# Performance work log

Hardware: AMD Instinct MI355X
Metric: run time of the kernel (lower is better)

Reference implementation:

```python
import jax, jax.numpy as jnp
import numpy as np

D = 69      # input_size = 54 dofs + 15 actions
E = 132     # time2vec embedding
R = 1024    # rnn_size
B = 2048    # batch
S = 50      # source_seq_len
T = 25      # target_seq_len


def setup_inputs() -> dict:
    key = jax.random.key(0)
    ks = jax.random.split(key, 18)
    w = lambda k, shape: jax.random.normal(k, shape, jnp.float32) * 0.05
    return dict(
        encoder_inputs=jax.random.normal(ks[0], (B, S - 1, D), jnp.float32),
        decoder_inputs=jax.random.normal(ks[1], (B, T, D), jnp.float32),
        noise=jax.random.normal(ks[2], (B, R), jnp.float32),
        Wih_enc=w(ks[3], (4 * R, D + E)), Whh_enc=w(ks[4], (4 * R, R)),
        bih_enc=w(ks[5], (4 * R,)), bhh_enc=w(ks[6], (4 * R,)),
        Wih_dec=w(ks[7], (4 * R, D)), Whh_dec=w(ks[8], (4 * R, R)),
        bih_dec=w(ks[9], (4 * R,)), bhh_dec=w(ks[10], (4 * R,)),
        fc1_w=w(ks[11], (D, R)), fc1_b=w(ks[12], (D,)),
        mu_w=w(ks[13], (1, R)), mu_b=w(ks[14], (1,)),
        sigma_w=w(ks[15], (1, R)), sigma_b=jnp.ones((1,), jnp.float32),  # bias 1 keeps sigma away from 0
        t2v_w=w(ks[16], (E, D)), t2v_b=w(ks[17], (E,)),
    )


def _lstm_step(x, h, c, Wih, Whh, bih, bhh):
    # PyTorch LSTMCell gate order: i, f, g, o
    gates = x @ Wih.T + bih + h @ Whh.T + bhh
    i, f, g, o = jnp.split(gates, 4, axis=-1)
    c = jax.nn.sigmoid(f) * c + jax.nn.sigmoid(i) * jnp.tanh(g)
    h = jax.nn.sigmoid(o) * jnp.tanh(c)
    return h, c


def _forward(encoder_inputs, decoder_inputs, noise,
             Wih_enc, Whh_enc, bih_enc, bhh_enc,
             Wih_dec, Whh_dec, bih_dec, bhh_dec,
             fc1_w, fc1_b, mu_w, mu_b, sigma_w, sigma_b, t2v_w, t2v_b):
    batch = encoder_inputs.shape[0]
    # time2vec embedding + concat: [B, S-1, D+E]
    emb = jnp.sin(encoder_inputs @ t2v_w.T + t2v_b)
    enc_seq = jnp.swapaxes(jnp.concatenate([encoder_inputs, emb], axis=2), 0, 1)
    h0 = jnp.zeros((batch, R), encoder_inputs.dtype)
    c0 = jnp.zeros((batch, R), encoder_inputs.dtype)

    def enc_step(carry, x):
        h, c = carry
        h, c = _lstm_step(x, h, c, Wih_enc, Whh_enc, bih_enc, bhh_enc)
        return (h, c), None  # dropout is identity in eval mode

    (h, c), _ = jax.lax.scan(enc_step, (h0, c0), enc_seq)

    mu = h @ mu_w.T + mu_b          # [B, 1]
    sigma = c @ sigma_w.T + sigma_b  # [B, 1]
    h = (h - mu) / sigma
    c = (c - mu) / sigma
    # eval-mode stochastic perturbation (same noise added to both, as in torch)
    h = h + 10.0 * noise
    c = c + 10.0 * noise

    dec_seq = jnp.swapaxes(decoder_inputs, 0, 1)  # [T, B, D]

    def dec_step(carry, x):
        h, c = carry
        h, c = _lstm_step(x, h, c, Wih_dec, Whh_dec, bih_dec, bhh_dec)
        out = x + h @ fc1_w.T + fc1_b  # residual projection
        return (h, c), out

    _, outs = jax.lax.scan(dec_step, (h, c), dec_seq)  # [T, B, D]
    return jnp.swapaxes(outs, 0, 1)  # [B, T, D]


def reference(encoder_inputs, decoder_inputs, noise,
              Wih_enc, Whh_enc, bih_enc, bhh_enc,
              Wih_dec, Whh_dec, bih_dec, bhh_dec,
              fc1_w, fc1_b, mu_w, mu_b, sigma_w, sigma_b, t2v_w, t2v_b):
    return _forward(encoder_inputs, decoder_inputs, noise,
                    Wih_enc, Whh_enc, bih_enc, bhh_enc,
                    Wih_dec, Whh_dec, bih_dec, bhh_dec,
                    fc1_w, fc1_b, mu_w, mu_b, sigma_w, sigma_b, t2v_w, t2v_b)
```

## Files before the change

### kernel.cpp

```cpp
#include <hip/hip_runtime.h>
#include <hip/hip_bf16.h>
#include <math.h>

#define DI 69
#define EE 132
#define RR 1024
#define BB 2048
#define TT 25
#define SE 49

typedef _Float16 f16;
typedef _Float16 v8h __attribute__((ext_vector_type(8)));
typedef float f32x4 __attribute__((ext_vector_type(4)));

__device__ __forceinline__ float sigm(float x) { return 1.0f / (1.0f + __expf(-x)); }
__device__ __forceinline__ float tanhf_fast(float x) {
  float e = __expf(2.0f * x);
  return 1.0f - 2.0f / (e + 1.0f);
}

typedef const __attribute__((address_space(1))) char* gas1p;
typedef __attribute__((address_space(3))) char* las3p;
__device__ __forceinline__ void gld16(const void* g, void* l) {
  __builtin_amdgcn_global_load_lds((gas1p)g, (las3p)l, 16, 0, 0);
}



__global__ void prep_misc_kernel(float* __restrict__ c, f16* __restrict__ h0,
                                 const float* __restrict__ bih_e, const float* __restrict__ bhh_e,
                                 const float* __restrict__ bih_d, const float* __restrict__ bhh_d,
                                 float* __restrict__ bias_e, float* __restrict__ bias_d,
                                 const float* __restrict__ fc1_w, f16* __restrict__ fc1h)
{
  int i = blockIdx.x * 256 + threadIdx.x;
  if (i < BB * RR) { c[i] = 0.0f; h0[i] = (f16)0.0f; }
  if (i < 4096) { bias_e[i] = bih_e[i] + bhh_e[i]; bias_d[i] = bih_d[i] + bhh_d[i]; }
  if (i < 128 * RR) {
    int dr = i >> 10, k = i & 1023;
    int kd = k ^ ((dr & 7) << 3);
    fc1h[(dr << 10) | kd] = (f16)((dr < DI) ? fc1_w[dr * RR + k] : 0.0f);
  }
}

__global__ void prep_wq_kernel(const float* __restrict__ Whh, const float* __restrict__ Wih,
                               f16* __restrict__ Wq, int KT, int DIN)
{
  int j = blockIdx.x;
  int xo = (j & 7) << 3;
  for (int k = threadIdx.x; k < KT; k += blockDim.x) {
    float v;
    if (k < RR) v = Whh[(size_t)j * RR + k];
    else { int kk = k - RR; v = (kk < DIN) ? Wih[(size_t)j * DIN + kk] : 0.0f; }
    Wq[(size_t)j * KT + (k ^ xo)] = (f16)v;
  }
}

__global__ __launch_bounds__(256)
void feat_enc_kernel(const float* __restrict__ enc_in,
                     const float* __restrict__ t2v_w, const float* __restrict__ t2v_b,
                     f16* __restrict__ feat)
{
  __shared__ float wl[132 * 100];
  __shared__ float xl[32 * 92];
  __shared__ float bl[132];
  const int tid = threadIdx.x;
  const int t = blockIdx.x >> 6;
  const int b0 = (blockIdx.x & 63) * 32;

  for (int i = tid; i < 132 * 18; i += 256) {
    int e = i / 18, s = i - e * 18, k = s * 4;
    const float* src = t2v_w + e * DI + k;
    float4 v;
    v.x = src[0];
    v.y = (k + 1 < DI) ? src[1] : 0.f;
    v.z = (k + 2 < DI) ? src[2] : 0.f;
    v.w = (k + 3 < DI) ? src[3] : 0.f;
    *(float4*)(wl + e * 100 + k) = v;
  }
  for (int i = tid; i < 32 * 18; i += 256) {
    int r = i / 18, s = i - r * 18, k = s * 4;
    const float* src = enc_in + ((size_t)(b0 + r) * SE + t) * DI + k;
    float4 v;
    v.x = src[0];
    v.y = (k + 1 < DI) ? src[1] : 0.f;
    v.z = (k + 2 < DI) ? src[2] : 0.f;
    v.w = (k + 3 < DI) ? src[3] : 0.f;
    *(float4*)(xl + r * 92 + k) = v;
  }
  if (tid < 132) bl[tid] = t2v_b[tid];
  __syncthreads();

  const int gr = tid >> 5, ge = tid & 31;
  float acc[4][4] = {};
  const float* xr = xl + (gr * 4) * 92;
  for (int k4 = 0; k4 < 18; ++k4) {
    float4 xv[4], wv[4];
    #pragma unroll
    for (int i = 0; i < 4; ++i) xv[i] = *(const float4*)(xr + i * 92 + k4 * 4);
    #pragma unroll
    for (int j = 0; j < 4; ++j) wv[j] = *(const float4*)(wl + (ge + 32 * j) * 100 + k4 * 4);
    #pragma unroll
    for (int i = 0; i < 4; ++i)
      #pragma unroll
      for (int j = 0; j < 4; ++j)
        acc[i][j] += xv[i].x * wv[j].x + xv[i].y * wv[j].y + xv[i].z * wv[j].z + xv[i].w * wv[j].w;
  }
  #pragma unroll
  for (int i = 0; i < 4; ++i) {
    int b = b0 + gr * 4 + i;
    size_t base = ((size_t)t * BB + b) * 256;
    int xo = (b & 7) << 3;
    #pragma unroll
    for (int j = 0; j < 4; ++j) {
      int e = ge + 32 * j;
      feat[base + ((69 + e) ^ xo)] = (f16)__sinf(acc[i][j] + bl[e]);
    }
  }
  if (tid < 32) {
    int b = b0 + tid;
    float a2[4] = {0.f, 0.f, 0.f, 0.f};
    for (int k4 = 0; k4 < 18; ++k4) {
      float4 xv = *(const float4*)(xl + tid * 92 + k4 * 4);
      #pragma unroll
      for (int j = 0; j < 4; ++j) {
        float4 wv = *(const float4*)(wl + (128 + j) * 100 + k4 * 4);
        a2[j] += xv.x * wv.x + xv.y * wv.y + xv.z * wv.z + xv.w * wv.w;
      }
    }
    size_t base = ((size_t)t * BB + b) * 256;
    int xo = (b & 7) << 3;
    #pragma unroll
    for (int j = 0; j < 4; ++j)
      feat[base + ((197 + j) ^ xo)] = (f16)__sinf(a2[j] + bl[128 + j]);
  }
  for (int i = tid; i < 32 * 256; i += 256) {
    int r = i >> 8, k = i & 255;
    if (k >= 69 && k < 201) continue;
    float v = (k < DI) ? xl[r * 92 + k] : 0.f;
    int b = b0 + r;
    feat[((size_t)t * BB + b) * 256 + (k ^ ((b & 7) << 3))] = (f16)v;
  }
}

__global__ void feat_dec_kernel(const float* __restrict__ dec_in, f16* __restrict__ feat)
{
  int idx = blockIdx.x * 256 + threadIdx.x;
  if (idx >= TT * BB * 128) return;
  int k = idx & 127;
  int r = idx >> 7;
  int t = r >> 11, b = r & (BB - 1);
  float v = (k < DI) ? dec_in[(size_t)b * TT * DI + t * DI + k] : 0.0f;
  feat[((size_t)r << 7) | (k ^ ((b & 7) << 3))] = (f16)v;
}

template<int FT, int FPAD, bool WF32>
__global__ __launch_bounds__(256, 2)
void lstm_step_kernel(const f16* __restrict__ hin, const f16* __restrict__ feat,
                      const f16* __restrict__ Wq, const float* __restrict__ bias,
                      float* __restrict__ c, f16* __restrict__ hout,
                      float* __restrict__ hf32)
{
  constexpr int KT = (16 + FT) * 64;
  __shared__ __align__(16) f16 lA[128 * 64];
  __shared__ __align__(16) f16 lB[128 * 64];
  const int tid = threadIdx.x;
  const int m0 = blockIdx.y * 128;
  const int u0 = blockIdx.x * 32;
  const int lane = tid & 63, w = tid >> 6;
  const int wm = w >> 1, wn = w & 1;
  const int lrow = lane & 15;
  const int r8 = lane >> 3, s8 = lane & 7;

  const f16* pA[4]; const f16* pB[4];
  f16* dA[4]; f16* dB[4];
  #pragma unroll
  for (int i = 0; i < 4; ++i) {
    int rA = w * 32 + 8 * i;
    dA[i] = lA + rA * 64;
    dB[i] = lB + rA * 64;
    pA[i] = hin + (size_t)(m0 + rA + r8) * RR + s8 * 8;
    pB[i] = Wq + (size_t)(w * 1024 + u0 + 8 * i + r8) * KT + s8 * 8;
  }

  f32x4 acc[4][4];
  #pragma unroll
  for (int a = 0; a < 4; ++a)
    #pragma unroll
    for (int g = 0; g < 4; ++g) acc[a][g] = (f32x4){0.f, 0.f, 0.f, 0.f};

  const int sw0 = (((lane >> 4)) ^ s8) * 8;
  const int sw1 = (((lane >> 4) | 4) ^ s8) * 8;
  const f16* a0 = lA + (wm * 64 + lrow) * 64 + sw0;
  const f16* a1 = lA + (wm * 64 + lrow) * 64 + sw1;
  const f16* b0 = lB + (wn * 16 + lrow) * 64 + sw0;
  const f16* b1 = lB + (wn * 16 + lrow) * 64 + sw1;

  for (int kt = 0; kt < 16 + FT; ++kt) {
    if (kt == 16) {
      #pragma unroll
      for (int i = 0; i < 4; ++i)
        pA[i] = feat + (size_t)(m0 + w * 32 + 8 * i + r8) * FPAD + s8 * 8;
    }
    #pragma unroll
    for (int i = 0; i < 4; ++i) { gld16(pA[i], dA[i]); pA[i] += 64; }
    #pragma unroll
    for (int i = 0; i < 4; ++i) { gld16(pB[i], dB[i]); pB[i] += 64; }
    __syncthreads();

    v8h av0[4], av1[4], bv0[4], bv1[4];
    #pragma unroll
    for (int mf = 0; mf < 4; ++mf) {
      av0[mf] = *(const v8h*)(a0 + mf * 1024);
      av1[mf] = *(const v8h*)(a1 + mf * 1024);
    }
    #pragma unroll
    for (int g = 0; g < 4; ++g) {
      bv0[g] = *(const v8h*)(b0 + g * 2048);
      bv1[g] = *(const v8h*)(b1 + g * 2048);
    }
    #pragma unroll
    for (int mf = 0; mf < 4; ++mf)
      #pragma unroll
      for (int g = 0; g < 4; ++g) {
        acc[mf][g] = __builtin_amdgcn_mfma_f32_16x16x32_f16(av0[mf], bv0[g], acc[mf][g], 0, 0, 0);
        acc[mf][g] = __builtin_amdgcn_mfma_f32_16x16x32_f16(av1[mf], bv1[g], acc[mf][g], 0, 0, 0);
      }
    __syncthreads();
  }

  const int u = u0 + wn * 16 + lrow;
  const float bi = bias[u], bf = bias[1024 + u], bg = bias[2048 + u], bo = bias[3072 + u];
  #pragma unroll
  for (int mf = 0; mf < 4; ++mf) {
    int rbase = m0 + wm * 64 + mf * 16 + (lane >> 4) * 4;
    #pragma unroll
    for (int q = 0; q < 4; ++q) {
      int r = rbase + q;
      size_t idxc = (size_t)r * RR + u;
      float iv = acc[mf][0][q] + bi;
      float fv = acc[mf][1][q] + bf;
      float gv = acc[mf][2][q] + bg;
      float ov = acc[mf][3][q] + bo;
      float cn = sigm(fv) * c[idxc] + sigm(iv) * tanhf_fast(gv);
      float hn = sigm(ov) * tanhf_fast(cn);
      c[idxc] = cn;
      hout[(size_t)r * RR + (u ^ ((r & 7) << 3))] = (f16)hn;
      if (WF32) hf32[idxc] = hn;
    }
  }
}

__global__ void musigma_kernel(const float* __restrict__ hf, float* __restrict__ c,
                               const float* __restrict__ noise,
                               const float* __restrict__ mu_w, const float* __restrict__ mu_b,
                               const float* __restrict__ sig_w, const float* __restrict__ sig_b,
                               f16* __restrict__ hout)
{
  int b = blockIdx.x, tid = threadIdx.x;
  __shared__ float red[8];
  __shared__ float musig[2];
  float sh = 0.f, sc = 0.f;
  for (int k = tid; k < RR; k += 256) {
    size_t idx = (size_t)b * RR + k;
    sh += hf[idx] * mu_w[k];
    sc += c[idx] * sig_w[k];
  }
  for (int off = 32; off > 0; off >>= 1) { sh += __shfl_down(sh, off); sc += __shfl_down(sc, off); }
  int wid = tid >> 6;
  if ((tid & 63) == 0) { red[wid] = sh; red[4 + wid] = sc; }
  __syncthreads();
  if (tid == 0) {
    musig[0] = red[0] + red[1] + red[2] + red[3] + mu_b[0];
    musig[1] = red[4] + red[5] + red[6] + red[7] + sig_b[0];
  }
  __syncthreads();
  float mu = musig[0], sg = musig[1];
  int xo = (b & 7) << 3;
  for (int k = tid; k < RR; k += 256) {
    size_t idx = (size_t)b * RR + k;
    float n10 = 10.0f * noise[idx];
    float hh = (hf[idx] - mu) / sg + n10;
    float cc = (c[idx] - mu) / sg + n10;
    hout[(size_t)b * RR + (k ^ xo)] = (f16)hh;
    c[idx] = cc;
  }
}

__global__ __launch_bounds__(256, 2)
void final_fc_kernel(const f16* __restrict__ Hd, const f16* __restrict__ fw,
                     const float* __restrict__ fb, const float* __restrict__ dec_in,
                     float* __restrict__ out)
{
  __shared__ __align__(16) f16 lA[128 * 64];
  __shared__ __align__(16) f16 lB[128 * 64];
  const int tid = threadIdx.x;
  const int m0 = blockIdx.x * 128;
  const int lane = tid & 63, w = tid >> 6;
  const int lrow = lane & 15;
  const int r8 = lane >> 3, s8 = lane & 7;

  const f16* pA[4]; const f16* pB[4];
  f16* dA[4]; f16* dB[4];
  #pragma unroll
  for (int i = 0; i < 4; ++i) {
    int rA = w * 32 + 8 * i;
    dA[i] = lA + rA * 64;
    dB[i] = lB + rA * 64;
    pA[i] = Hd + (size_t)(m0 + rA + r8) * RR + s8 * 8;
    pB[i] = fw + (size_t)(rA + r8) * RR + s8 * 8;
  }

  f32x4 acc[2][5];
  #pragma unroll
  for (int a = 0; a < 2; ++a)
    #pragma unroll
    for (int n = 0; n < 5; ++n) acc[a][n] = (f32x4){0.f, 0.f, 0.f, 0.f};

  const int sw0 = (((lane >> 4)) ^ s8) * 8;
  const int sw1 = (((lane >> 4) | 4) ^ s8) * 8;
  const f16* a0 = lA + (w * 32 + lrow) * 64 + sw0;
  const f16* a1 = lA + (w * 32 + lrow) * 64 + sw1;
  const f16* b0 = lB + lrow * 64 + sw0;
  const f16* b1 = lB + lrow * 64 + sw1;

  for (int kt = 0; kt < 16; ++kt) {
    #pragma unroll
    for (int i = 0; i < 4; ++i) { gld16(pA[i], dA[i]); pA[i] += 64; }
    #pragma unroll
    for (int i = 0; i < 4; ++i) { gld16(pB[i], dB[i]); pB[i] += 64; }
    __syncthreads();
    v8h av0[2], av1[2], bv0[5], bv1[5];
    #pragma unroll
    for (int mf = 0; mf < 2; ++mf) {
      av0[mf] = *(const v8h*)(a0 + mf * 1024);
      av1[mf] = *(const v8h*)(a1 + mf * 1024);
    }
    #pragma unroll
    for (int nf = 0; nf < 5; ++nf) {
      bv0[nf] = *(const v8h*)(b0 + nf * 1024);
      bv1[nf] = *(const v8h*)(b1 + nf * 1024);
    }
    #pragma unroll
    for (int mf = 0; mf < 2; ++mf)
      #pragma unroll
      for (int nf = 0; nf < 5; ++nf) {
        acc[mf][nf] = __builtin_amdgcn_mfma_f32_16x16x32_f16(av0[mf], bv0[nf], acc[mf][nf], 0, 0, 0);
        acc[mf][nf] = __builtin_amdgcn_mfma_f32_16x16x32_f16(av1[mf], bv1[nf], acc[mf][nf], 0, 0, 0);
      }
    __syncthreads();
  }
  #pragma unroll
  for (int mf = 0; mf < 2; ++mf) {
    int rbase = m0 + w * 32 + mf * 16 + (lane >> 4) * 4;
    #pragma unroll
    for (int nf = 0; nf < 5; ++nf) {
      int col = nf * 16 + lrow;
      if (col < DI) {
        #pragma unroll
        for (int q = 0; q < 4; ++q) {
          int m = rbase + q;
          int t = m >> 11, b = m & (BB - 1);
          size_t oi = (size_t)b * TT * DI + t * DI + col;
          out[oi] = acc[mf][nf][q] + fb[col] + dec_in[oi];
        }
      }
    }
  }
}

extern "C" void kernel_launch(void* const* d_in, const int* in_sizes, int n_in,
                              void* d_out, int out_size, void* d_ws, size_t ws_size,
                              hipStream_t stream)
{
  const float* enc_in = (const float*)d_in[0];
  const float* dec_in = (const float*)d_in[1];
  const float* noise  = (const float*)d_in[2];
  const float* Wih_e  = (const float*)d_in[3];
  const float* Whh_e  = (const float*)d_in[4];
  const float* bih_e  = (const float*)d_in[5];
  const float* bhh_e  = (const float*)d_in[6];
  const float* Wih_d  = (const float*)d_in[7];
  const float* Whh_d  = (const float*)d_in[8];
  const float* bih_d  = (const float*)d_in[9];
  const float* bhh_d  = (const float*)d_in[10];
  const float* fc1_w  = (const float*)d_in[11];
  const float* fc1_b  = (const float*)d_in[12];
  const float* mu_w   = (const float*)d_in[13];
  const float* mu_b   = (const float*)d_in[14];
  const float* sig_w  = (const float*)d_in[15];
  const float* sig_b  = (const float*)d_in[16];
  const float* t2v_w  = (const float*)d_in[17];
  const float* t2v_b  = (const float*)d_in[18];
  float* outp = (float*)d_out;

  char* ws = (char*)d_ws;
  size_t off = 0;
  auto alloc = [&](size_t bytes) -> char* {
    char* p = ws + off; off += (bytes + 255) & ~(size_t)255; return p;
  };
  f16*   wq_e   = (f16*)alloc((size_t)4096 * 1280 * 2);
  f16*   wq_d   = (f16*)alloc((size_t)4096 * 1152 * 2);
  f16*   fc1h   = (f16*)alloc((size_t)128 * RR * 2);
  float* bias_e = (float*)alloc(4096 * 4);
  float* bias_d = (float*)alloc(4096 * 4);
  f16*   feat_e = (f16*)alloc((size_t)SE * BB * 256 * 2);
  f16*   feat_d = (f16*)alloc((size_t)TT * BB * 128 * 2);
  f16*   h_ping = (f16*)alloc((size_t)BB * RR * 2);
  f16*   h_pong = (f16*)alloc((size_t)BB * RR * 2);
  float* cbuf   = (float*)alloc((size_t)BB * RR * 4);
  float* hf32   = (float*)alloc((size_t)BB * RR * 4);
  f16*   Hd     = (f16*)alloc((size_t)TT * BB * RR * 2);
  if (off > ws_size) return;

  prep_misc_kernel<<<(BB * RR + 255) / 256, 256, 0, stream>>>(
      cbuf, h_ping, bih_e, bhh_e, bih_d, bhh_d, bias_e, bias_d, fc1_w, fc1h);
  prep_wq_kernel<<<4096, 256, 0, stream>>>(Whh_e, Wih_e, wq_e, 1280, DI + EE);
  prep_wq_kernel<<<4096, 256, 0, stream>>>(Whh_d, Wih_d, wq_d, 1152, DI);
  feat_enc_kernel<<<SE * (BB / 32), 256, 0, stream>>>(enc_in, t2v_w, t2v_b, feat_e);
  feat_dec_kernel<<<(TT * BB * 128 + 255) / 256, 256, 0, stream>>>(dec_in, feat_d);

  dim3 sgrid(32, 16, 1);

  f16* hcur = h_ping; f16* hnxt = h_pong;
  for (int t = 0; t < SE; ++t) {
    const f16* ft = feat_e + (size_t)t * BB * 256;
    if (t == SE - 1)
      lstm_step_kernel<4, 256, true><<<sgrid, 256, 0, stream>>>(
          hcur, ft, wq_e, bias_e, cbuf, hnxt, hf32);
    else
      lstm_step_kernel<4, 256, false><<<sgrid, 256, 0, stream>>>(
          hcur, ft, wq_e, bias_e, cbuf, hnxt, nullptr);
    f16* tmp = hcur; hcur = hnxt; hnxt = tmp;
  }

  musigma_kernel<<<BB, 256, 0, stream>>>(hf32, cbuf, noise, mu_w, mu_b, sig_w, sig_b, h_ping);

  const f16* din = h_ping;
  for (int t = 0; t < TT; ++t) {
    f16* hout = Hd + (size_t)t * BB * RR;
    lstm_step_kernel<2, 128, false><<<sgrid, 256, 0, stream>>>(
        din, feat_d + (size_t)t * BB * 128, wq_d, bias_d, cbuf, hout, nullptr);
    din = hout;
  }

  final_fc_kernel<<<(TT * BB) / 128, 256, 0, stream>>>(Hd, fc1h, fc1_b, dec_in, outp);
}
```

Baseline: 2.407 ms.

## Double-buffer LDS tiles in LSTM/fc1 GEMMs and move time2vec onto MFMA

```diff
diff --git a/kernel.cpp b/kernel.cpp
--- a/kernel.cpp
+++ b/kernel.cpp
@@ -31,7 +31,8 @@
                                  const float* __restrict__ bih_e, const float* __restrict__ bhh_e,
                                  const float* __restrict__ bih_d, const float* __restrict__ bhh_d,
                                  float* __restrict__ bias_e, float* __restrict__ bias_d,
-                                 const float* __restrict__ fc1_w, f16* __restrict__ fc1h)
+                                 const float* __restrict__ fc1_w, f16* __restrict__ fc1h,
+                                 const float* __restrict__ t2v_w, f16* __restrict__ wt2)
 {
   int i = blockIdx.x * 256 + threadIdx.x;
   if (i < BB * RR) { c[i] = 0.0f; h0[i] = (f16)0.0f; }
@@ -41,6 +42,11 @@
     int kd = k ^ ((dr & 7) << 3);
     fc1h[(dr << 10) | kd] = (f16)((dr < DI) ? fc1_w[dr * RR + k] : 0.0f);
   }
+  if (i < 160 * 128) {
+    int r = i >> 7, k = i & 127;
+    float v = (r < EE && k < DI) ? t2v_w[r * DI + k] : 0.0f;
+    wt2[(r << 7) | (k ^ ((r & 7) << 3))] = (f16)v;
+  }
 }
 
 __global__ void prep_wq_kernel(const float* __restrict__ Whh, const float* __restrict__ Wih,
@@ -56,90 +62,91 @@
   }
 }
 
+__global__ void xf16_kernel(const float* __restrict__ enc_in,
+                            f16* __restrict__ Xf, f16* __restrict__ feat)
+{
+  int idx = blockIdx.x * 256 + threadIdx.x;
+  if (idx >= SE * BB * 256) return;
+  int j = idx & 255, row = idx >> 8;
+  int t = row >> 11, b = row & (BB - 1);
+  int xo = (b & 7) << 3;
+  int k = j ^ xo;
+  if (k < 128) {
+    float v = (k < DI) ? enc_in[(size_t)b * SE * DI + t * DI + k] : 0.0f;
+    Xf[(size_t)row * 128 + j] = (f16)v;
+    if (k < DI) feat[(size_t)row * 256 + j] = (f16)v;
+  } else if (k >= 201) {
+    feat[(size_t)row * 256 + j] = (f16)0.0f;
+  }
+}
+
 __global__ __launch_bounds__(256)
-void feat_enc_kernel(const float* __restrict__ enc_in,
-                     const float* __restrict__ t2v_w, const float* __restrict__ t2v_b,
-                     f16* __restrict__ feat)
-{
-  __shared__ float wl[132 * 100];
-  __shared__ float xl[32 * 92];
-  __shared__ float bl[132];
+void t2v_kernel(const f16* __restrict__ Xf, const f16* __restrict__ wt2,
+                const float* __restrict__ t2v_b, f16* __restrict__ feat)
+{
+  __shared__ __align__(16) f16 lA[128 * 64];
+  __shared__ __align__(16) f16 lB[160 * 64];
+  __shared__ float bl[EE];
   const int tid = threadIdx.x;
-  const int t = blockIdx.x >> 6;
-  const int b0 = (blockIdx.x & 63) * 32;
-
-  for (int i = tid; i < 132 * 18; i += 256) {
-    int e = i / 18, s = i - e * 18, k = s * 4;
-    const float* src = t2v_w + e * DI + k;
-    float4 v;
-    v.x = src[0];
-    v.y = (k + 1 < DI) ? src[1] : 0.f;
-    v.z = (k + 2 < DI) ? src[2] : 0.f;
-    v.w = (k + 3 < DI) ? src[3] : 0.f;
-    *(float4*)(wl + e * 100 + k) = v;
-  }
-  for (int i = tid; i < 32 * 18; i += 256) {
-    int r = i / 18, s = i - r * 18, k = s * 4;
-    const float* src = enc_in + ((size_t)(b0 + r) * SE + t) * DI + k;
-    float4 v;
-    v.x = src[0];
-    v.y = (k + 1 < DI) ? src[1] : 0.f;
-    v.z = (k + 2 < DI) ? src[2] : 0.f;
-    v.w = (k + 3 < DI) ? src[3] : 0.f;
-    *(float4*)(xl + r * 92 + k) = v;
-  }
-  if (tid < 132) bl[tid] = t2v_b[tid];
-  __syncthreads();
-
-  const int gr = tid >> 5, ge = tid & 31;
-  float acc[4][4] = {};
-  const float* xr = xl + (gr * 4) * 92;
-  for (int k4 = 0; k4 < 18; ++k4) {
-    float4 xv[4], wv[4];
-    #pragma unroll
-    for (int i = 0; i < 4; ++i) xv[i] = *(const float4*)(xr + i * 92 + k4 * 4);
-    #pragma unroll
-    for (int j = 0; j < 4; ++j) wv[j] = *(const float4*)(wl + (ge + 32 * j) * 100 + k4 * 4);
+  const int m0 = blockIdx.x * 128;
+  const int lane = tid & 63, w = tid >> 6;
+  const int lrow = lane & 15;
+  const int r8 = lane >> 3, s8 = lane & 7;
+  if (tid < EE) bl[tid] = t2v_b[tid];
+
+  f32x4 acc[2][10];
+  #pragma unroll
+  for (int a = 0; a < 2; ++a)
+    #pragma unroll
+    for (int n = 0; n < 10; ++n) acc[a][n] = (f32x4){0.f, 0.f, 0.f, 0.f};
+
+  const int sw0 = (((lane >> 4)) ^ s8) * 8;
+  const int sw1 = (((lane >> 4) | 4) ^ s8) * 8;
+
+  for (int kt = 0; kt < 2; ++kt) {
+    __syncthreads();
     #pragma unroll
     for (int i = 0; i < 4; ++i)
-      #pragma unroll
-      for (int j = 0; j < 4; ++j)
-        acc[i][j] += xv[i].x * wv[j].x + xv[i].y * wv[j].y + xv[i].z * wv[j].z + xv[i].w * wv[j].w;
-  }
-  #pragma unroll
-  for (int i = 0; i < 4; ++i) {
-    int b = b0 + gr * 4 + i;
-    size_t base = ((size_t)t * BB + b) * 256;
-    int xo = (b & 7) << 3;
-    #pragma unroll
-    for (int j = 0; j < 4; ++j) {
-      int e = ge + 32 * j;
-      feat[base + ((69 + e) ^ xo)] = (f16)__sinf(acc[i][j] + bl[e]);
-    }
-  }
-  if (tid < 32) {
-    int b = b0 + tid;
-    float a2[4] = {0.f, 0.f, 0.f, 0.f};
-    for (int k4 = 0; k4 < 18; ++k4) {
-      float4 xv = *(const float4*)(xl + tid * 92 + k4 * 4);
-      #pragma unroll
-      for (int j = 0; j < 4; ++j) {
-        float4 wv = *(const float4*)(wl + (128 + j) * 100 + k4 * 4);
-        a2[j] += xv.x * wv.x + xv.y * wv.y + xv.z * wv.z + xv.w * wv.w;
-      }
-    }
-    size_t base = ((size_t)t * BB + b) * 256;
-    int xo = (b & 7) << 3;
-    #pragma unroll
-    for (int j = 0; j < 4; ++j)
-      feat[base + ((197 + j) ^ xo)] = (f16)__sinf(a2[j] + bl[128 + j]);
-  }
-  for (int i = tid; i < 32 * 256; i += 256) {
-    int r = i >> 8, k = i & 255;
-    if (k >= 69 && k < 201) continue;
-    float v = (k < DI) ? xl[r * 92 + k] : 0.f;
-    int b = b0 + r;
-    feat[((size_t)t * BB + b) * 256 + (k ^ ((b & 7) << 3))] = (f16)v;
+      gld16(Xf + (size_t)(m0 + w * 32 + 8 * i + r8) * 128 + kt * 64 + s8 * 8,
+            &lA[(w * 32 + 8 * i) * 64]);
+    #pragma unroll
+    for (int i = 0; i < 5; ++i)
+      gld16(wt2 + (size_t)(w * 40 + 8 * i + r8) * 128 + kt * 64 + s8 * 8,
+            &lB[(w * 40 + 8 * i) * 64]);
+    __syncthreads();
+    v8h av0[2], av1[2];
+    #pragma unroll
+    for (int mf = 0; mf < 2; ++mf) {
+      av0[mf] = *(const v8h*)(&lA[(w * 32 + mf * 16 + lrow) * 64 + sw0]);
+      av1[mf] = *(const v8h*)(&lA[(w * 32 + mf * 16 + lrow) * 64 + sw1]);
+    }
+    #pragma unroll
+    for (int nf = 0; nf < 10; ++nf) {
+      v8h bv0 = *(const v8h*)(&lB[(nf * 16 + lrow) * 64 + sw0]);
+      v8h bv1 = *(const v8h*)(&lB[(nf * 16 + lrow) * 64 + sw1]);
+      #pragma unroll
+      for (int mf = 0; mf < 2; ++mf) {
+        acc[mf][nf] = __builtin_amdgcn_mfma_f32_16x16x32_f16(av0[mf], bv0, acc[mf][nf], 0, 0, 0);
+        acc[mf][nf] = __builtin_amdgcn_mfma_f32_16x16x32_f16(av1[mf], bv1, acc[mf][nf], 0, 0, 0);
+      }
+    }
+  }
+  #pragma unroll
+  for (int nf = 0; nf < 10; ++nf) {
+    int e = nf * 16 + lrow;
+    if (e < EE) {
+      float be = bl[e];
+      #pragma unroll
+      for (int mf = 0; mf < 2; ++mf) {
+        int rbase = m0 + w * 32 + mf * 16 + (lane >> 4) * 4;
+        #pragma unroll
+        for (int q = 0; q < 4; ++q) {
+          int row = rbase + q;
+          feat[(size_t)row * 256 + ((69 + e) ^ ((row & 7) << 3))]
+              = (f16)__sinf(acc[mf][nf][q] + be);
+        }
+      }
+    }
   }
 }
 
@@ -161,9 +168,10 @@
                       float* __restrict__ c, f16* __restrict__ hout,
                       float* __restrict__ hf32)
 {
-  constexpr int KT = (16 + FT) * 64;
-  __shared__ __align__(16) f16 lA[128 * 64];
-  __shared__ __align__(16) f16 lB[128 * 64];
+  constexpr int NIT = 16 + FT;
+  constexpr int KT = NIT * 64;
+  __shared__ __align__(16) f16 lA[2][128 * 64];
+  __shared__ __align__(16) f16 lB[2][128 * 64];
   const int tid = threadIdx.x;
   const int m0 = blockIdx.y * 128;
   const int u0 = blockIdx.x * 32;
@@ -173,13 +181,11 @@
   const int r8 = lane >> 3, s8 = lane & 7;
 
   const f16* pA[4]; const f16* pB[4];
-  f16* dA[4]; f16* dB[4];
+  int rA[4];
   #pragma unroll
   for (int i = 0; i < 4; ++i) {
-    int rA = w * 32 + 8 * i;
-    dA[i] = lA + rA * 64;
-    dB[i] = lB + rA * 64;
-    pA[i] = hin + (size_t)(m0 + rA + r8) * RR + s8 * 8;
+    rA[i] = w * 32 + 8 * i;
+    pA[i] = hin + (size_t)(m0 + rA[i] + r8) * RR + s8 * 8;
     pB[i] = Wq + (size_t)(w * 1024 + u0 + 8 * i + r8) * KT + s8 * 8;
   }
 
@@ -191,33 +197,41 @@
 
   const int sw0 = (((lane >> 4)) ^ s8) * 8;
   const int sw1 = (((lane >> 4) | 4) ^ s8) * 8;
-  const f16* a0 = lA + (wm * 64 + lrow) * 64 + sw0;
-  const f16* a1 = lA + (wm * 64 + lrow) * 64 + sw1;
-  const f16* b0 = lB + (wn * 16 + lrow) * 64 + sw0;
-  const f16* b1 = lB + (wn * 16 + lrow) * 64 + sw1;
-
-  for (int kt = 0; kt < 16 + FT; ++kt) {
-    if (kt == 16) {
-      #pragma unroll
-      for (int i = 0; i < 4; ++i)
-        pA[i] = feat + (size_t)(m0 + w * 32 + 8 * i + r8) * FPAD + s8 * 8;
-    }
-    #pragma unroll
-    for (int i = 0; i < 4; ++i) { gld16(pA[i], dA[i]); pA[i] += 64; }
-    #pragma unroll
-    for (int i = 0; i < 4; ++i) { gld16(pB[i], dB[i]); pB[i] += 64; }
+  const int oa = (wm * 64 + lrow) * 64;
+  const int ob = (wn * 16 + lrow) * 64;
+
+  #pragma unroll
+  for (int i = 0; i < 4; ++i) { gld16(pA[i], &lA[0][rA[i] * 64]); pA[i] += 64; }
+  #pragma unroll
+  for (int i = 0; i < 4; ++i) { gld16(pB[i], &lB[0][rA[i] * 64]); pB[i] += 64; }
+
+  int cur = 0;
+  for (int kt = 0; kt < NIT; ++kt) {
     __syncthreads();
-
+    if (kt + 1 < NIT) {
+      if (kt + 1 == 16) {
+        #pragma unroll
+        for (int i = 0; i < 4; ++i)
+          pA[i] = feat + (size_t)(m0 + rA[i] + r8) * FPAD + s8 * 8;
+      }
+      int nb = cur ^ 1;
+      #pragma unroll
+      for (int i = 0; i < 4; ++i) { gld16(pA[i], &lA[nb][rA[i] * 64]); pA[i] += 64; }
+      #pragma unroll
+      for (int i = 0; i < 4; ++i) { gld16(pB[i], &lB[nb][rA[i] * 64]); pB[i] += 64; }
+    }
+    const f16* Ab = &lA[cur][oa];
+    const f16* Bb = &lB[cur][ob];
     v8h av0[4], av1[4], bv0[4], bv1[4];
     #pragma unroll
     for (int mf = 0; mf < 4; ++mf) {
-      av0[mf] = *(const v8h*)(a0 + mf * 1024);
-      av1[mf] = *(const v8h*)(a1 + mf * 1024);
+      av0[mf] = *(const v8h*)(Ab + mf * 1024 + sw0);
+      av1[mf] = *(const v8h*)(Ab + mf * 1024 + sw1);
     }
     #pragma unroll
     for (int g = 0; g < 4; ++g) {
-      bv0[g] = *(const v8h*)(b0 + g * 2048);
-      bv1[g] = *(const v8h*)(b1 + g * 2048);
+      bv0[g] = *(const v8h*)(Bb + g * 2048 + sw0);
+      bv1[g] = *(const v8h*)(Bb + g * 2048 + sw1);
     }
     #pragma unroll
     for (int mf = 0; mf < 4; ++mf)
@@ -226,7 +240,7 @@
         acc[mf][g] = __builtin_amdgcn_mfma_f32_16x16x32_f16(av0[mf], bv0[g], acc[mf][g], 0, 0, 0);
         acc[mf][g] = __builtin_amdgcn_mfma_f32_16x16x32_f16(av1[mf], bv1[g], acc[mf][g], 0, 0, 0);
       }
-    __syncthreads();
+    cur ^= 1;
   }
 
   const int u = u0 + wn * 16 + lrow;
@@ -292,8 +306,8 @@
                      const float* __restrict__ fb, const float* __restrict__ dec_in,
                      float* __restrict__ out)
 {
-  __shared__ __align__(16) f16 lA[128 * 64];
-  __shared__ __align__(16) f16 lB[128 * 64];
+  __shared__ __align__(16) f16 lA[2][128 * 64];
+  __shared__ __align__(16) f16 lB[2][128 * 64];
   const int tid = threadIdx.x;
   const int m0 = blockIdx.x * 128;
   const int lane = tid & 63, w = tid >> 6;
@@ -301,14 +315,12 @@
   const int r8 = lane >> 3, s8 = lane & 7;
 
   const f16* pA[4]; const f16* pB[4];
-  f16* dA[4]; f16* dB[4];
+  int rA[4];
   #pragma unroll
   for (int i = 0; i < 4; ++i) {
-    int rA = w * 32 + 8 * i;
-    dA[i] = lA + rA * 64;
-    dB[i] = lB + rA * 64;
-    pA[i] = Hd + (size_t)(m0 + rA + r8) * RR + s8 * 8;
-    pB[i] = fw + (size_t)(rA + r8) * RR + s8 * 8;
+    rA[i] = w * 32 + 8 * i;
+    pA[i] = Hd + (size_t)(m0 + rA[i] + r8) * RR + s8 * 8;
+    pB[i] = fw + (size_t)(rA[i] + r8) * RR + s8 * 8;
   }
 
   f32x4 acc[2][5];
@@ -319,27 +331,36 @@
 
   const int sw0 = (((lane >> 4)) ^ s8) * 8;
   const int sw1 = (((lane >> 4) | 4) ^ s8) * 8;
-  const f16* a0 = lA + (w * 32 + lrow) * 64 + sw0;
-  const f16* a1 = lA + (w * 32 + lrow) * 64 + sw1;
-  const f16* b0 = lB + lrow * 64 + sw0;
-  const f16* b1 = lB + lrow * 64 + sw1;
-
+  const int oa = (w * 32 + lrow) * 64;
+  const int ob = lrow * 64;
+
+  #pragma unroll
+  for (int i = 0; i < 4; ++i) { gld16(pA[i], &lA[0][rA[i] * 64]); pA[i] += 64; }
+  #pragma unroll
+  for (int i = 0; i < 4; ++i) { gld16(pB[i], &lB[0][rA[i] * 64]); pB[i] += 64; }
+
+  int cur = 0;
   for (int kt = 0; kt < 16; ++kt) {
-    #pragma unroll
-    for (int i = 0; i < 4; ++i) { gld16(pA[i], dA[i]); pA[i] += 64; }
-    #pragma unroll
-    for (int i = 0; i < 4; ++i) { gld16(pB[i], dB[i]); pB[i] += 64; }
     __syncthreads();
+    if (kt + 1 < 16) {
+      int nb = cur ^ 1;
+      #pragma unroll
+      for (int i = 0; i < 4; ++i) { gld16(pA[i], &lA[nb][rA[i] * 64]); pA[i] += 64; }
+      #pragma unroll
+      for (int i = 0; i < 4; ++i) { gld16(pB[i], &lB[nb][rA[i] * 64]); pB[i] += 64; }
+    }
+    const f16* Ab = &lA[cur][oa];
+    const f16* Bb = &lB[cur][ob];
     v8h av0[2], av1[2], bv0[5], bv1[5];
     #pragma unroll
     for (int mf = 0; mf < 2; ++mf) {
-      av0[mf] = *(const v8h*)(a0 + mf * 1024);
-      av1[mf] = *(const v8h*)(a1 + mf * 1024);
+      av0[mf] = *(const v8h*)(Ab + mf * 1024 + sw0);
+      av1[mf] = *(const v8h*)(Ab + mf * 1024 + sw1);
     }
     #pragma unroll
     for (int nf = 0; nf < 5; ++nf) {
-      bv0[nf] = *(const v8h*)(b0 + nf * 1024);
-      bv1[nf] = *(const v8h*)(b1 + nf * 1024);
+      bv0[nf] = *(const v8h*)(Bb + nf * 1024 + sw0);
+      bv1[nf] = *(const v8h*)(Bb + nf * 1024 + sw1);
     }
     #pragma unroll
     for (int mf = 0; mf < 2; ++mf)
@@ -348,7 +369,7 @@
         acc[mf][nf] = __builtin_amdgcn_mfma_f32_16x16x32_f16(av0[mf], bv0[nf], acc[mf][nf], 0, 0, 0);
         acc[mf][nf] = __builtin_amdgcn_mfma_f32_16x16x32_f16(av1[mf], bv1[nf], acc[mf][nf], 0, 0, 0);
       }
-    __syncthreads();
+    cur ^= 1;
   }
   #pragma unroll
   for (int mf = 0; mf < 2; ++mf) {
@@ -402,6 +423,7 @@
   f16*   wq_e   = (f16*)alloc((size_t)4096 * 1280 * 2);
   f16*   wq_d   = (f16*)alloc((size_t)4096 * 1152 * 2);
   f16*   fc1h   = (f16*)alloc((size_t)128 * RR * 2);
+  f16*   wt2    = (f16*)alloc((size_t)160 * 128 * 2);
   float* bias_e = (float*)alloc(4096 * 4);
   float* bias_d = (float*)alloc(4096 * 4);
   f16*   feat_e = (f16*)alloc((size_t)SE * BB * 256 * 2);
@@ -412,12 +434,14 @@
   float* hf32   = (float*)alloc((size_t)BB * RR * 4);
   f16*   Hd     = (f16*)alloc((size_t)TT * BB * RR * 2);
   if (off > ws_size) return;
+  f16*   Xf     = Hd;
 
   prep_misc_kernel<<<(BB * RR + 255) / 256, 256, 0, stream>>>(
-      cbuf, h_ping, bih_e, bhh_e, bih_d, bhh_d, bias_e, bias_d, fc1_w, fc1h);
+      cbuf, h_ping, bih_e, bhh_e, bih_d, bhh_d, bias_e, bias_d, fc1_w, fc1h, t2v_w, wt2);
   prep_wq_kernel<<<4096, 256, 0, stream>>>(Whh_e, Wih_e, wq_e, 1280, DI + EE);
   prep_wq_kernel<<<4096, 256, 0, stream>>>(Whh_d, Wih_d, wq_d, 1152, DI);
-  feat_enc_kernel<<<SE * (BB / 32), 256, 0, stream>>>(enc_in, t2v_w, t2v_b, feat_e);
+  xf16_kernel<<<(SE * BB * 256 + 255) / 256, 256, 0, stream>>>(enc_in, Xf, feat_e);
+  t2v_kernel<<<SE * (BB / 128), 256, 0, stream>>>(Xf, wt2, t2v_b, feat_e);
   feat_dec_kernel<<<(TT * BB * 128 + 255) / 256, 256, 0, stream>>>(dec_in, feat_d);
 
   dim3 sgrid(32, 16, 1);
```

New measurement: 2.721 ms. +13.0%, slower.
